# Kernel tuning notes

Hardware: AMD Instinct MI355X
Metric: run time of the kernel (lower is better)

Reference implementation:

```python
import jax, jax.numpy as jnp
import numpy as np

N_NODES = 100000
N_EDGES = 1000000
NEG_SLOPE = 0.2


def gat_conv(x, src, dst, W, al, ar, b, res, activation):
    """DGL-style GATConv. res is None (no residual), 'id' (identity residual), or a [in,H*D] matrix."""
    H, D = al.shape
    n = x.shape[0]
    feat = (x @ W).reshape(n, H, D)                      # [N,H,D]
    el = jnp.einsum('nhd,hd->nh', feat, al)              # [N,H]
    er = jnp.einsum('nhd,hd->nh', feat, ar)              # [N,H]
    e = jax.nn.leaky_relu(el[src] + er[dst], NEG_SLOPE)  # [E,H]
    # edge softmax over incoming edges of each dst node
    m = jax.lax.stop_gradient(jax.ops.segment_max(e, dst, num_segments=n))
    ex = jnp.exp(e - m[dst])
    s = jax.ops.segment_sum(ex, dst, num_segments=n)
    alpha = ex / s[dst]                                  # [E,H]
    out = jax.ops.segment_sum(feat[src] * alpha[:, :, None], dst, num_segments=n)  # [N,H,D]
    if res == 'id':
        out = out + x.reshape(n, H, D)
    elif res is not None:
        out = out + (x @ res).reshape(n, H, D)
    out = out + b.reshape(1, H, D)
    if activation is not None:
        out = activation(out)
    return out


def setup_inputs() -> dict:
    key = jax.random.key(0)
    ks = jax.random.split(key, 20)
    F_IN, HID = 128, 32
    H1, H2, H3 = 4, 4, 1
    C = 40
    sc = 0.1
    inp = {
        'x':   jax.random.normal(ks[0], (N_NODES, F_IN), dtype=jnp.float32),
        'src': jax.random.randint(ks[1], (N_EDGES,), 0, N_NODES, dtype=jnp.int32),
        'dst': jax.random.randint(ks[2], (N_EDGES,), 0, N_NODES, dtype=jnp.int32),
        # layer 1: in=128 -> H1*HID=128, no residual, elu
        'W1':  sc * jax.random.normal(ks[3], (F_IN, H1 * HID), dtype=jnp.float32),
        'al1': sc * jax.random.normal(ks[4], (H1, HID), dtype=jnp.float32),
        'ar1': sc * jax.random.normal(ks[5], (H1, HID), dtype=jnp.float32),
        'b1':  jnp.zeros((H1 * HID,), dtype=jnp.float32),
        # layer 2: in=128 -> H2*HID=128, identity residual, elu
        'W2':  sc * jax.random.normal(ks[6], (H1 * HID, H2 * HID), dtype=jnp.float32),
        'al2': sc * jax.random.normal(ks[7], (H2, HID), dtype=jnp.float32),
        'ar2': sc * jax.random.normal(ks[8], (H2, HID), dtype=jnp.float32),
        'b2':  jnp.zeros((H2 * HID,), dtype=jnp.float32),
        # layer 3 (output): in=128 -> H3*HID=32, projected residual, no activation
        'W3':  sc * jax.random.normal(ks[9], (H2 * HID, H3 * HID), dtype=jnp.float32),
        'al3': sc * jax.random.normal(ks[10], (H3, HID), dtype=jnp.float32),
        'ar3': sc * jax.random.normal(ks[11], (H3, HID), dtype=jnp.float32),
        'b3':  jnp.zeros((H3 * HID,), dtype=jnp.float32),
        'res3': sc * jax.random.normal(ks[12], (H2 * HID, H3 * HID), dtype=jnp.float32),
        # final classifier
        'Wfc': sc * jax.random.normal(ks[13], (HID, C), dtype=jnp.float32),
        'bfc': jnp.zeros((C,), dtype=jnp.float32),
    }
    return inp


def reference(x, src, dst, W1, al1, ar1, b1, W2, al2, ar2, b2, W3, al3, ar3, b3, res3, Wfc, bfc):
    n = x.shape[0]
    h = gat_conv(x, src, dst, W1, al1, ar1, b1, None, jax.nn.elu).reshape(n, -1)   # [N, 128]
    h = gat_conv(h, src, dst, W2, al2, ar2, b2, 'id', jax.nn.elu).reshape(n, -1)   # [N, 128]
    h = gat_conv(h, src, dst, W3, al3, ar3, b3, res3, None).mean(axis=1)           # [N, 32]
    return h @ Wfc + bfc                                                           # [N, 40]
```

## Files before the change

### kernel.cpp

```cpp
#include <hip/hip_runtime.h>
#include <cstdint>
#include <cstddef>

#define NN 100000
#define NE 1000000
#define GEMM_BLOCKS 1563
#define GEMM2_BLOCKS 782
#define TICKET4_BLOCKS 977
#define NB_SCAN 391
#define LOG2E 1.4426950408896340736f

typedef unsigned int uint;
typedef unsigned short ushort;
typedef __attribute__((ext_vector_type(8))) short bfrag;
typedef __attribute__((ext_vector_type(4))) float f32x4;

__device__ __forceinline__ ushort f2bf(float f){
  uint u = __float_as_uint(f);
  u += 0x7fffu + ((u >> 16) & 1u);
  return (ushort)(u >> 16);
}
__device__ __forceinline__ float bflo(uint p){ return __uint_as_float(p << 16); }
__device__ __forceinline__ float bfhi(uint p){ return __uint_as_float(p & 0xffff0000u); }


__device__ __forceinline__ void bfrag_body(const float* __restrict__ B1, const float* __restrict__ B2,
                                           int n1, int n2, int NT, ushort* __restrict__ out, int i){
  if (i >= NT*4*64) return;
  int l = i & 63, ks = (i>>6)&3, nt = i>>8;
  int col = nt*16 + (l&15);
  int k0  = ks*32 + (l>>4)*8;
  const float* B; int stride, c;
  if (col < n1){ B = B1; stride = n1; c = col; }
  else         { B = B2; stride = n2; c = col - n1; }
  ushort v[8];
  #pragma unroll
  for (int j=0;j<8;j++) v[j] = f2bf(B[(size_t)(k0+j)*stride + c]);
  uint4 pk;
  pk.x = (uint)v[0] | ((uint)v[1]<<16);
  pk.y = (uint)v[2] | ((uint)v[3]<<16);
  pk.z = (uint)v[4] | ((uint)v[5]<<16);
  pk.w = (uint)v[6] | ((uint)v[7]<<16);
  *(uint4*)(out + (size_t)i*8) = pk;
}

__global__ __launch_bounds__(256) void k_packs(const float* __restrict__ W1, const float* __restrict__ W2,
                                               const float* __restrict__ W3, const float* __restrict__ res3,
                                               ushort* __restrict__ Bf1, ushort* __restrict__ Bf2,
                                               ushort* __restrict__ Bf3){
  int r = blockIdx.x, t = threadIdx.x;
  if (r < 8)       bfrag_body(W1, nullptr, 128, 0, 8, Bf1, r*256 + t);
  else if (r < 16) bfrag_body(W2, nullptr, 128, 0, 8, Bf2, (r-8)*256 + t);
  else             bfrag_body(W3, res3,    32, 32, 4, Bf3, (r-16)*256 + t);
}


__global__ __launch_bounds__(256, 4)
void k_gemm1_ticket(const float* __restrict__ x, const ushort* __restrict__ Bf1,
                    ushort* __restrict__ featb,
                    const float* __restrict__ al, const float* __restrict__ ar,
                    float* __restrict__ el, float* __restrict__ er,
                    const int* __restrict__ dst, int* __restrict__ cnt4, int* __restrict__ tick){
  int bid = blockIdx.x, t = threadIdx.x;
  if (bid >= GEMM_BLOCKS){
    int idx = (bid - GEMM_BLOCKS)*256 + t;
    if (idx < NE/4){
      int e0 = idx*4;
      int4 d4 = *(const int4*)(dst + e0);
      int t0 = atomicAdd(&cnt4[(uint)d4.x*4u + 0u], 1);
      int t1 = atomicAdd(&cnt4[(uint)d4.y*4u + 1u], 1);
      int t2 = atomicAdd(&cnt4[(uint)d4.z*4u + 2u], 1);
      int t3 = atomicAdd(&cnt4[(uint)d4.w*4u + 3u], 1);
      *(int4*)(tick + e0) = make_int4(t0,t1,t2,t3);
    }
    return;
  }

  int l = t & 63, w = t >> 6;
  int rw = bid*64 + w*16;
  int c = l & 15, g = l >> 4;

  f32x4 acc[8];
  #pragma unroll
  for (int nt=0;nt<8;nt++) acc[nt] = (f32x4){0.f,0.f,0.f,0.f};

  int rowA = rw + c; if (rowA >= NN) rowA = NN-1;
  const float* Ap = x + (size_t)rowA*128 + g*8;
  const bfrag* Bp = (const bfrag*)Bf1;

  #pragma unroll
  for (int ks=0; ks<4; ++ks){
    float4 f0 = *(const float4*)(Ap + ks*32);
    float4 f1 = *(const float4*)(Ap + ks*32 + 4);
    bfrag a;
    a[0]=(short)f2bf(f0.x); a[1]=(short)f2bf(f0.y); a[2]=(short)f2bf(f0.z); a[3]=(short)f2bf(f0.w);
    a[4]=(short)f2bf(f1.x); a[5]=(short)f2bf(f1.y); a[6]=(short)f2bf(f1.z); a[7]=(short)f2bf(f1.w);
    #pragma unroll
    for (int nt=0; nt<8; ++nt){
      bfrag b = Bp[(nt*4+ks)*64 + l];
      acc[nt] = __builtin_amdgcn_mfma_f32_16x16x32_bf16(a, b, acc[nt], 0, 0, 0);
    }
  }

  float alv[4][2], arv[4][2];
  #pragma unroll
  for (int h=0;h<4;h++){
    alv[h][0]=al[h*32+c]*LOG2E;    arv[h][0]=ar[h*32+c]*LOG2E;
    alv[h][1]=al[h*32+16+c]*LOG2E; arv[h][1]=ar[h*32+16+c]*LOG2E;
  }

  #pragma unroll
  for (int reg=0; reg<4; ++reg){
    int row = rw + g*4 + reg;
    bool ok = row < NN;
    #pragma unroll
    for (int h=0;h<4;h++){
      float pl = acc[2*h][reg]*alv[h][0] + acc[2*h+1][reg]*alv[h][1];
      float pr = acc[2*h][reg]*arv[h][0] + acc[2*h+1][reg]*arv[h][1];
      #pragma unroll
      for (int off=1; off<16; off<<=1){ pl += __shfl_xor(pl,off); pr += __shfl_xor(pr,off); }
      if (ok && c==0){ el[(size_t)row*4 + h] = pl; er[(size_t)row*4 + h] = pr; }
    }
    if (ok){
      #pragma unroll
      for (int nt=0; nt<8; ++nt)
        featb[(size_t)row*128 + nt*16 + c] = f2bf(acc[nt][reg]);
    }
  }
}


__global__ __launch_bounds__(256) void k_scan_local(const int* __restrict__ cnt4, int* __restrict__ shoff,
                                                    int* __restrict__ rowptr, int* __restrict__ bsum){
  __shared__ int sm[256];
  int t = threadIdx.x;
  int i = blockIdx.x*256 + t;
  int v = 0;
  if (i < NN){
    int4 cc = ((const int4*)cnt4)[i];
    v = cc.x + cc.y + cc.z + cc.w;
    int4 so;
    so.x = 0; so.y = cc.x; so.z = cc.x + cc.y; so.w = cc.x + cc.y + cc.z;
    ((int4*)shoff)[i] = so;
  }
  sm[t] = v;
  __syncthreads();
  for (int off=1; off<256; off<<=1){
    int u = (t>=off) ? sm[t-off] : 0;
    __syncthreads();
    sm[t] += u;
    __syncthreads();
  }
  if (i < NN) rowptr[i] = sm[t] - v;
  if (t == 255) bsum[blockIdx.x] = sm[255];
}

__global__ __launch_bounds__(512) void k_scan_finish(int* __restrict__ rowptr, const int* __restrict__ bsum){
  __shared__ int sm[512];
  __shared__ int ex[512];
  int t = threadIdx.x;
  int v = (t < NB_SCAN) ? bsum[t] : 0;
  sm[t] = v;
  __syncthreads();
  for (int off=1; off<512; off<<=1){
    int u = (t>=off) ? sm[t-off] : 0;
    __syncthreads();
    sm[t] += u;
    __syncthreads();
  }
  ex[t] = sm[t] - v;
  __syncthreads();
  int i = blockIdx.x*512 + t;
  if (i < NN) rowptr[i] += ex[i>>8];
  else if (i == NN) rowptr[NN] = NE;
}


__global__ __launch_bounds__(256) void k_dhist(const int* __restrict__ rowptr, int* __restrict__ dbin){
  __shared__ int lh[256];
  int t = threadIdx.x;
  lh[t] = 0;
  __syncthreads();
  int n = blockIdx.x*256 + t;
  if (n < NN){
    int deg = rowptr[n+1] - rowptr[n];
    atomicAdd(&lh[deg > 255 ? 255 : deg], 1);
  }
  __syncthreads();
  if (lh[t] > 0) atomicAdd(&dbin[t], lh[t]);
}

__global__ __launch_bounds__(256) void k_dscan(int* __restrict__ dbin){
  __shared__ int sm[256];
  int t = threadIdx.x;
  int v = dbin[t];
  sm[t] = v;
  __syncthreads();
  for (int off=1; off<256; off<<=1){
    int u = (t>=off) ? sm[t-off] : 0;
    __syncthreads();
    sm[t] += u;
    __syncthreads();
  }
  dbin[t] = sm[t] - v;
}

__global__ __launch_bounds__(256) void k_place_dscat(const int* __restrict__ src, const int* __restrict__ dst,
                                                     const int* __restrict__ rowptr, const int* __restrict__ shoff,
                                                     const int* __restrict__ tick, int* __restrict__ csr,
                                                     int* __restrict__ dbin, int* __restrict__ perm){
  int bid = blockIdx.x, t = threadIdx.x;
  if (bid < TICKET4_BLOCKS){
    int idx = bid*256 + t;
    if (idx < NE/4){
      int e0 = idx*4;
      int4 s4 = *(const int4*)(src + e0);
      int4 d4 = *(const int4*)(dst + e0);
      int4 t4 = *(const int4*)(tick + e0);
      csr[rowptr[d4.x] + shoff[(uint)d4.x*4u + 0u] + t4.x] = s4.x;
      csr[rowptr[d4.y] + shoff[(uint)d4.y*4u + 1u] + t4.y] = s4.y;
      csr[rowptr[d4.z] + shoff[(uint)d4.z*4u + 2u] + t4.z] = s4.z;
      csr[rowptr[d4.w] + shoff[(uint)d4.w*4u + 3u] + t4.w] = s4.w;
    }
  } else {
    __shared__ int lh[256];
    __shared__ int lbase[256];
    lh[t] = 0;
    __syncthreads();
    int n = (bid - TICKET4_BLOCKS)*256 + t;
    int bin = -1, lticket = 0;
    if (n < NN){
      int deg = rowptr[n+1] - rowptr[n];
      bin = deg > 255 ? 255 : deg;
      lticket = atomicAdd(&lh[bin], 1);
    }
    __syncthreads();
    if (lh[t] > 0) lbase[t] = atomicAdd(&dbin[t], lh[t]);
    __syncthreads();
    if (n < NN) perm[lbase[bin] + lticket] = n;
  }
}


template<int NT, int NTF, int H>
__global__ __launch_bounds__(512) void k_gemm_mfma(const ushort* __restrict__ Ab, const ushort* __restrict__ Bf,
                                                   ushort* __restrict__ featb, float* __restrict__ Cres,
                                                   const float* __restrict__ al, const float* __restrict__ ar,
                                                   float* __restrict__ el, float* __restrict__ er, int M){
  __shared__ ushort Bs[NT*2048];
  int t = threadIdx.x;
  #pragma unroll
  for (int i=0; i<NT/2; ++i)
    ((uint4*)Bs)[i*512 + t] = ((const uint4*)Bf)[i*512 + t];
  __syncthreads();

  int l = t & 63, w = t >> 6;
  int rw = blockIdx.x*128 + w*16;
  int c = l & 15, g = l >> 4;

  f32x4 acc[NT];
  #pragma unroll
  for (int nt=0;nt<NT;nt++) acc[nt] = (f32x4){0.f,0.f,0.f,0.f};

  int rowA = rw + c; if (rowA >= M) rowA = M-1;
  const ushort* Ap = Ab + (size_t)rowA*128 + g*8;
  const bfrag* Bp = (const bfrag*)Bs;

  #pragma unroll
  for (int ks=0; ks<4; ++ks){
    bfrag a = *(const bfrag*)(Ap + ks*32);
    #pragma unroll
    for (int nt=0; nt<NT; ++nt){
      bfrag b = Bp[(nt*4+ks)*64 + l];
      acc[nt] = __builtin_amdgcn_mfma_f32_16x16x32_bf16(a, b, acc[nt], 0, 0, 0);
    }
  }

  float alv[H][2], arv[H][2];
  #pragma unroll
  for (int h=0;h<H;h++){
    alv[h][0]=al[h*32+c]*LOG2E;    arv[h][0]=ar[h*32+c]*LOG2E;
    alv[h][1]=al[h*32+16+c]*LOG2E; arv[h][1]=ar[h*32+16+c]*LOG2E;
  }

  #pragma unroll
  for (int reg=0; reg<4; ++reg){
    int row = rw + g*4 + reg;
    bool ok = row < M;
    #pragma unroll
    for (int h=0;h<H;h++){
      float pl = acc[2*h][reg]*alv[h][0] + acc[2*h+1][reg]*alv[h][1];
      float pr = acc[2*h][reg]*arv[h][0] + acc[2*h+1][reg]*arv[h][1];
      #pragma unroll
      for (int off=1; off<16; off<<=1){ pl += __shfl_xor(pl,off); pr += __shfl_xor(pr,off); }
      if (ok && c==0){ el[(size_t)row*H + h] = pl; er[(size_t)row*H + h] = pr; }
    }
    if (ok){
      #pragma unroll
      for (int nt=0; nt<NTF; ++nt)
        featb[(size_t)row*(NTF*16) + nt*16 + c] = f2bf(acc[nt][reg]);
      #pragma unroll
      for (int nt=NTF; nt<NT; ++nt)
        Cres[(size_t)row*((NT-NTF)*16) + (nt-NTF)*16 + c] = acc[nt][reg];
    }
  }
}


template<int RK>
__global__ __launch_bounds__(256) void k_agg4(const int* __restrict__ rowptr, const int* __restrict__ csr,
                                              const int* __restrict__ perm,
                                              const ushort* __restrict__ feat,
                                              const float* __restrict__ el, const float* __restrict__ er,
                                              const void* __restrict__ res, const float* __restrict__ bias,
                                              ushort* __restrict__ out, int act){
  int t = threadIdx.x;
  int l15 = t & 15;
  int node = perm[blockIdx.x*16 + (t>>4)];

  int beg = rowptr[node], deg = rowptr[node+1] - beg;
  int hm = l15 >> 2;
  float erh = er[(size_t)node*4 + hm];
  const int* cp = csr + beg;
  uint fo = (uint)l15*8u;

  float ssum = 0.f;
  float a0=0.f,a1=0.f,a2=0.f,a3=0.f,a4=0.f,a5=0.f,a6=0.f,a7=0.f;

  int ei = 0;
  for (; ei+4 <= deg; ei += 4){
    int s0 = cp[ei], s1 = cp[ei+1], s2 = cp[ei+2], s3 = cp[ei+3];
    uint4 p0 = *(const uint4*)(feat + ((uint)s0*128u + fo));
    uint4 p1 = *(const uint4*)(feat + ((uint)s1*128u + fo));
    uint4 p2 = *(const uint4*)(feat + ((uint)s2*128u + fo));
    uint4 p3 = *(const uint4*)(feat + ((uint)s3*128u + fo));
    float v0 = el[(uint)s0*4u + hm] + erh; v0 = fmaxf(v0, 0.2f*v0);
    float v1 = el[(uint)s1*4u + hm] + erh; v1 = fmaxf(v1, 0.2f*v1);
    float v2 = el[(uint)s2*4u + hm] + erh; v2 = fmaxf(v2, 0.2f*v2);
    float v3 = el[(uint)s3*4u + hm] + erh; v3 = fmaxf(v3, 0.2f*v3);
    float w0 = __builtin_amdgcn_exp2f(v0);
    float w1 = __builtin_amdgcn_exp2f(v1);
    float w2 = __builtin_amdgcn_exp2f(v2);
    float w3 = __builtin_amdgcn_exp2f(v3);
    ssum += (w0 + w1) + (w2 + w3);
    a0 += w0*bflo(p0.x) + w1*bflo(p1.x) + w2*bflo(p2.x) + w3*bflo(p3.x);
    a1 += w0*bfhi(p0.x) + w1*bfhi(p1.x) + w2*bfhi(p2.x) + w3*bfhi(p3.x);
    a2 += w0*bflo(p0.y) + w1*bflo(p1.y) + w2*bflo(p2.y) + w3*bflo(p3.y);
    a3 += w0*bfhi(p0.y) + w1*bfhi(p1.y) + w2*bfhi(p2.y) + w3*bfhi(p3.y);
    a4 += w0*bflo(p0.z) + w1*bflo(p1.z) + w2*bflo(p2.z) + w3*bflo(p3.z);
    a5 += w0*bfhi(p0.z) + w1*bfhi(p1.z) + w2*bfhi(p2.z) + w3*bfhi(p3.z);
    a6 += w0*bflo(p0.w) + w1*bflo(p1.w) + w2*bflo(p2.w) + w3*bflo(p3.w);
    a7 += w0*bfhi(p0.w) + w1*bfhi(p1.w) + w2*bfhi(p2.w) + w3*bfhi(p3.w);
  }
  for (; ei < deg; ++ei){
    int s0 = cp[ei];
    uint4 p0 = *(const uint4*)(feat + ((uint)s0*128u + fo));
    float v0 = el[(uint)s0*4u + hm] + erh; v0 = fmaxf(v0, 0.2f*v0);
    float w0 = __builtin_amdgcn_exp2f(v0);
    ssum += w0;
    a0 += w0*bflo(p0.x); a1 += w0*bfhi(p0.x);
    a2 += w0*bflo(p0.y); a3 += w0*bfhi(p0.y);
    a4 += w0*bflo(p0.z); a5 += w0*bfhi(p0.z);
    a6 += w0*bflo(p0.w); a7 += w0*bfhi(p0.w);
  }

  float inv = (deg > 0) ? 1.f/ssum : 0.f;
  float o0=a0*inv, o1=a1*inv, o2=a2*inv, o3=a3*inv;
  float o4=a4*inv, o5=a5*inv, o6=a6*inv, o7=a7*inv;
  if (RK == 1){
    uint4 rv = *(const uint4*)((const ushort*)res + (size_t)node*128 + fo);
    o0 += bflo(rv.x); o1 += bfhi(rv.x); o2 += bflo(rv.y); o3 += bfhi(rv.y);
    o4 += bflo(rv.z); o5 += bfhi(rv.z); o6 += bflo(rv.w); o7 += bfhi(rv.w);
  }
  float4 bv0 = *(const float4*)(bias + l15*8);
  float4 bv1 = *(const float4*)(bias + l15*8 + 4);
  o0 += bv0.x; o1 += bv0.y; o2 += bv0.z; o3 += bv0.w;
  o4 += bv1.x; o5 += bv1.y; o6 += bv1.z; o7 += bv1.w;
  if (act){
    o0 = (o0>0.f)?o0:__expf(o0)-1.f;
    o1 = (o1>0.f)?o1:__expf(o1)-1.f;
    o2 = (o2>0.f)?o2:__expf(o2)-1.f;
    o3 = (o3>0.f)?o3:__expf(o3)-1.f;
    o4 = (o4>0.f)?o4:__expf(o4)-1.f;
    o5 = (o5>0.f)?o5:__expf(o5)-1.f;
    o6 = (o6>0.f)?o6:__expf(o6)-1.f;
    o7 = (o7>0.f)?o7:__expf(o7)-1.f;
  }
  uint4 pk;
  pk.x = (uint)f2bf(o0) | ((uint)f2bf(o1)<<16);
  pk.y = (uint)f2bf(o2) | ((uint)f2bf(o3)<<16);
  pk.z = (uint)f2bf(o4) | ((uint)f2bf(o5)<<16);
  pk.w = (uint)f2bf(o6) | ((uint)f2bf(o7)<<16);
  *(uint4*)(out + (size_t)node*128 + fo) = pk;
}


__global__ __launch_bounds__(256) void k_agg1(const int* __restrict__ rowptr, const int* __restrict__ csr,
                                              const int* __restrict__ perm,
                                              const ushort* __restrict__ feat,
                                              const float* __restrict__ el, const float* __restrict__ er,
                                              const float* __restrict__ res, const float* __restrict__ bias,
                                              float* __restrict__ h3){
  int t = threadIdx.x;
  int l7 = t & 7;
  int node = perm[blockIdx.x*32 + (t>>3)];

  int beg = rowptr[node], deg = rowptr[node+1] - beg;
  float er0 = er[node];
  const int* cp = csr + beg;
  uint fo = (uint)l7*4u;

  float ssum = 0.f, a0=0.f, a1=0.f, a2=0.f, a3=0.f;
  int ei = 0;
  for (; ei+2 <= deg; ei += 2){
    int s0 = cp[ei], s1 = cp[ei+1];
    uint2 p0 = *(const uint2*)(feat + ((uint)s0*32u + fo));
    uint2 p1 = *(const uint2*)(feat + ((uint)s1*32u + fo));
    float v0 = el[s0] + er0; v0 = fmaxf(v0, 0.2f*v0);
    float v1 = el[s1] + er0; v1 = fmaxf(v1, 0.2f*v1);
    float w0 = __builtin_amdgcn_exp2f(v0);
    float w1 = __builtin_amdgcn_exp2f(v1);
    ssum += w0 + w1;
    a0 += w0*bflo(p0.x) + w1*bflo(p1.x);
    a1 += w0*bfhi(p0.x) + w1*bfhi(p1.x);
    a2 += w0*bflo(p0.y) + w1*bflo(p1.y);
    a3 += w0*bfhi(p0.y) + w1*bfhi(p1.y);
  }
  if (ei < deg){
    int s0 = cp[ei];
    uint2 p0 = *(const uint2*)(feat + ((uint)s0*32u + fo));
    float v0 = el[s0] + er0; v0 = fmaxf(v0, 0.2f*v0);
    float w0 = __builtin_amdgcn_exp2f(v0);
    ssum += w0;
    a0 += w0*bflo(p0.x); a1 += w0*bfhi(p0.x);
    a2 += w0*bflo(p0.y); a3 += w0*bfhi(p0.y);
  }

  float inv = (deg > 0) ? 1.f/ssum : 0.f;
  float4 rv = *(const float4*)(res + (size_t)node*32 + fo);
  float4 bv = *(const float4*)(bias + fo);
  float4 ov;
  ov.x = a0*inv + rv.x + bv.x;
  ov.y = a1*inv + rv.y + bv.y;
  ov.z = a2*inv + rv.z + bv.z;
  ov.w = a3*inv + rv.w + bv.w;
  *(float4*)(h3 + (size_t)node*32 + fo) = ov;
}


__global__ __launch_bounds__(256) void k_fc(const float* __restrict__ h, const float* __restrict__ W,
                                            const float* __restrict__ b, float* __restrict__ out){
  __shared__ float Ws[32*40];
  __shared__ float Hs[64][33];
  __shared__ float bs[40];
  int t = threadIdx.x;
  for (int i=t; i<1280; i+=256) Ws[i] = W[i];
  if (t < 40) bs[t] = b[t];
  int n0 = blockIdx.x*64;
  for (int idx=t; idx<512; idx+=256){
    int r = idx>>3, c4 = idx&7;
    float4 v;
    if (n0 + r < NN) v = *(const float4*)(h + (size_t)(n0+r)*32 + c4*4);
    else v = make_float4(0.f,0.f,0.f,0.f);
    Hs[r][c4*4+0]=v.x; Hs[r][c4*4+1]=v.y; Hs[r][c4*4+2]=v.z; Hs[r][c4*4+3]=v.w;
  }
  __syncthreads();
  int n = t>>2, cg = t&3;
  float acc[10];
  #pragma unroll
  for (int j=0;j<10;j++) acc[j] = 0.f;
  #pragma unroll
  for (int k=0;k<32;k++){
    float hv = Hs[n][k];
    #pragma unroll
    for (int j=0;j<10;j++) acc[j] += hv * Ws[k*40 + cg + 4*j];
  }
  int row = n0 + n;
  if (row < NN){
    #pragma unroll
    for (int j=0;j<10;j++) out[(size_t)row*40 + cg + 4*j] = acc[j] + bs[cg+4*j];
  }
}


extern "C" void kernel_launch(void* const* d_in, const int* in_sizes, int n_in,
                              void* d_out, int out_size, void* d_ws, size_t ws_size,
                              hipStream_t stream){
  const float* x    = (const float*)d_in[0];
  const int*   src  = (const int*)  d_in[1];
  const int*   dst  = (const int*)  d_in[2];
  const float* W1   = (const float*)d_in[3];
  const float* al1  = (const float*)d_in[4];
  const float* ar1  = (const float*)d_in[5];
  const float* b1   = (const float*)d_in[6];
  const float* W2   = (const float*)d_in[7];
  const float* al2  = (const float*)d_in[8];
  const float* ar2  = (const float*)d_in[9];
  const float* b2   = (const float*)d_in[10];
  const float* W3   = (const float*)d_in[11];
  const float* al3  = (const float*)d_in[12];
  const float* ar3  = (const float*)d_in[13];
  const float* b3   = (const float*)d_in[14];
  const float* res3 = (const float*)d_in[15];
  const float* Wfc  = (const float*)d_in[16];
  const float* bfc  = (const float*)d_in[17];
  float* out = (float*)d_out;

  char* ws = (char*)d_ws;
  size_t o = 0;
  auto alloc = [&](size_t bytes)->char*{
    char* p = ws + o;
    o += (bytes + 255) & ~(size_t)255;
    return p;
  };
  int*    rowptr = (int*)   alloc((size_t)(NN+1)*4);
  int*    cnt4   = (int*)   alloc((size_t)NN*4*4);
  int*    shoff  = (int*)   alloc((size_t)NN*4*4);
  int*    bsum   = (int*)   alloc(512*4);
  int*    dbin   = (int*)   alloc(256*4);
  int*    perm   = (int*)   alloc((size_t)NN*4);
  int*    tick   = (int*)   alloc((size_t)NE*4);
  int*    csr    = (int*)   alloc((size_t)NE*4);
  float*  el     = (float*) alloc((size_t)NN*4*4);
  float*  er     = (float*) alloc((size_t)NN*4*4);
  ushort* featb  = (ushort*)alloc((size_t)NN*128*2);
  ushort* h1b    = (ushort*)alloc((size_t)NN*128*2);
  ushort* h2b    = (ushort*)alloc((size_t)NN*128*2);
  float*  res3p  = (float*) alloc((size_t)NN*32*4);
  float*  h3     = (float*) alloc((size_t)NN*32*4);
  ushort* Bf1    = (ushort*)alloc((size_t)8*4*64*8*2);
  ushort* Bf2    = (ushort*)alloc((size_t)8*4*64*8*2);
  ushort* Bf3    = (ushort*)alloc((size_t)4*4*64*8*2);
  (void)ws_size; (void)n_in; (void)in_sizes; (void)out_size;

  hipMemsetAsync(cnt4, 0, (size_t)NN*4*4, stream);
  hipMemsetAsync(dbin, 0, 256*4, stream);

  k_packs<<<20, 256, 0, stream>>>(W1, W2, W3, res3, Bf1, Bf2, Bf3);

  k_gemm1_ticket<<<GEMM_BLOCKS+TICKET4_BLOCKS, 256, 0, stream>>>(x, Bf1, featb, al1, ar1, el, er,
                                                                 dst, cnt4, tick);

  k_scan_local<<<NB_SCAN, 256, 0, stream>>>(cnt4, shoff, rowptr, bsum);
  k_scan_finish<<<(NN+1+511)/512, 512, 0, stream>>>(rowptr, bsum);

  k_dhist<<<NB_SCAN, 256, 0, stream>>>(rowptr, dbin);
  k_dscan<<<1, 256, 0, stream>>>(dbin);
  k_place_dscat<<<TICKET4_BLOCKS+NB_SCAN, 256, 0, stream>>>(src, dst, rowptr, shoff, tick, csr,
                                                            dbin, perm);

  k_agg4<0><<<NN/16, 256, 0, stream>>>(rowptr, csr, perm, featb, el, er, nullptr, b1, h1b, 1);

  k_gemm_mfma<8,8,4><<<GEMM2_BLOCKS, 512, 0, stream>>>(h1b, Bf2, featb, nullptr, al2, ar2, el, er, NN);
  k_agg4<1><<<NN/16, 256, 0, stream>>>(rowptr, csr, perm, featb, el, er, h1b, b2, h2b, 1);

  k_gemm_mfma<4,2,1><<<GEMM2_BLOCKS, 512, 0, stream>>>(h2b, Bf3, featb, res3p, al3, ar3, el, er, NN);
  k_agg1<<<NN/32, 256, 0, stream>>>(rowptr, csr, perm, featb, el, er, res3p, b3, h3);
  k_fc<<<GEMM_BLOCKS, 256, 0, stream>>>(h3, Wfc, bfc, out);
}
```

Baseline: 298.0 us.

## Fold memsets and degree histogram into neighboring kernels, interleave ticket blocks with GEMM

Replaces the two memsets with zeroing blocks in the weight-packing kernel, and computes the degree histogram inside the local scan. The histogram scan runs as an extra block of the scan-finish kernel, removing four launches. The ticket-counting blocks are interleaved with the GEMM blocks and now handle one edge per thread instead of four, so atomics overlap with MFMA work. The risk is more blocks with less work each, and scalar dst loads in place of vectorized ones.

```diff
diff --git a/kernel.cpp b/kernel.cpp
--- a/kernel.cpp
+++ b/kernel.cpp
@@ -5,9 +5,12 @@
 #define NN 100000
 #define NE 1000000
 #define GEMM_BLOCKS 1563
+#define TICKET_BLOCKS 3907
+#define MERGED_BLOCKS 5470
 #define GEMM2_BLOCKS 782
 #define TICKET4_BLOCKS 977
 #define NB_SCAN 391
+#define NF_SCAN 196
 #define LOG2E 1.4426950408896340736f
 
 typedef unsigned int uint;
@@ -44,14 +47,21 @@
   *(uint4*)(out + (size_t)i*8) = pk;
 }
 
-__global__ __launch_bounds__(256) void k_packs(const float* __restrict__ W1, const float* __restrict__ W2,
+__global__ __launch_bounds__(256) void k_prep0(const float* __restrict__ W1, const float* __restrict__ W2,
                                                const float* __restrict__ W3, const float* __restrict__ res3,
                                                ushort* __restrict__ Bf1, ushort* __restrict__ Bf2,
-                                               ushort* __restrict__ Bf3){
+                                               ushort* __restrict__ Bf3,
+                                               int* __restrict__ cnt4, int* __restrict__ dbin){
   int r = blockIdx.x, t = threadIdx.x;
   if (r < 8)       bfrag_body(W1, nullptr, 128, 0, 8, Bf1, r*256 + t);
   else if (r < 16) bfrag_body(W2, nullptr, 128, 0, 8, Bf2, (r-8)*256 + t);
-  else             bfrag_body(W3, res3,    32, 32, 4, Bf3, (r-16)*256 + t);
+  else if (r < 20) bfrag_body(W3, res3,    32, 32, 4, Bf3, (r-16)*256 + t);
+  else if (r < 20 + NB_SCAN){
+    int i = (r-20)*256 + t;
+    if (i < NN) ((int4*)cnt4)[i] = make_int4(0,0,0,0);
+  } else {
+    dbin[t] = 0;
+  }
 }
 
 
@@ -61,20 +71,16 @@
                     const float* __restrict__ al, const float* __restrict__ ar,
                     float* __restrict__ el, float* __restrict__ er,
                     const int* __restrict__ dst, int* __restrict__ cnt4, int* __restrict__ tick){
-  int bid = blockIdx.x, t = threadIdx.x;
-  if (bid >= GEMM_BLOCKS){
-    int idx = (bid - GEMM_BLOCKS)*256 + t;
-    if (idx < NE/4){
-      int e0 = idx*4;
-      int4 d4 = *(const int4*)(dst + e0);
-      int t0 = atomicAdd(&cnt4[(uint)d4.x*4u + 0u], 1);
-      int t1 = atomicAdd(&cnt4[(uint)d4.y*4u + 1u], 1);
-      int t2 = atomicAdd(&cnt4[(uint)d4.z*4u + 2u], 1);
-      int t3 = atomicAdd(&cnt4[(uint)d4.w*4u + 3u], 1);
-      *(int4*)(tick + e0) = make_int4(t0,t1,t2,t3);
-    }
+  long b = blockIdx.x;
+  int t = threadIdx.x;
+  int g_lo = (int)( b      * GEMM_BLOCKS / MERGED_BLOCKS);
+  int g_hi = (int)((b + 1) * GEMM_BLOCKS / MERGED_BLOCKS);
+  if (g_hi == g_lo){
+    int e = (int)(b - g_lo)*256 + t;
+    if (e < NE) tick[e] = atomicAdd(&cnt4[(uint)dst[e]*4u + (e & 3)], 1);
     return;
   }
+  int bid = g_lo;
 
   int l = t & 63, w = t >> 6;
   int rw = bid*64 + w*16;
@@ -97,8 +103,8 @@
     a[4]=(short)f2bf(f1.x); a[5]=(short)f2bf(f1.y); a[6]=(short)f2bf(f1.z); a[7]=(short)f2bf(f1.w);
     #pragma unroll
     for (int nt=0; nt<8; ++nt){
-      bfrag b = Bp[(nt*4+ks)*64 + l];
-      acc[nt] = __builtin_amdgcn_mfma_f32_16x16x32_bf16(a, b, acc[nt], 0, 0, 0);
+      bfrag bb = Bp[(nt*4+ks)*64 + l];
+      acc[nt] = __builtin_amdgcn_mfma_f32_16x16x32_bf16(a, bb, acc[nt], 0, 0, 0);
     }
   }
 
@@ -131,9 +137,12 @@
 
 
 __global__ __launch_bounds__(256) void k_scan_local(const int* __restrict__ cnt4, int* __restrict__ shoff,
-                                                    int* __restrict__ rowptr, int* __restrict__ bsum){
+                                                    int* __restrict__ rowptr, int* __restrict__ bsum,
+                                                    int* __restrict__ dbin){
   __shared__ int sm[256];
-  int t = threadIdx.x;
+  __shared__ int lh[256];
+  int t = threadIdx.x;
+  lh[t] = 0;
   int i = blockIdx.x*256 + t;
   int v = 0;
   if (i < NN){
@@ -145,6 +154,7 @@
   }
   sm[t] = v;
   __syncthreads();
+  if (i < NN) atomicAdd(&lh[v > 255 ? 255 : v], 1);
   for (int off=1; off<256; off<<=1){
     int u = (t>=off) ? sm[t-off] : 0;
     __syncthreads();
@@ -153,12 +163,29 @@
   }
   if (i < NN) rowptr[i] = sm[t] - v;
   if (t == 255) bsum[blockIdx.x] = sm[255];
-}
-
-__global__ __launch_bounds__(512) void k_scan_finish(int* __restrict__ rowptr, const int* __restrict__ bsum){
+  __syncthreads();
+  if (lh[t] > 0) atomicAdd(&dbin[t], lh[t]);
+}
+
+
+__global__ __launch_bounds__(512) void k_scan_finish(int* __restrict__ rowptr, const int* __restrict__ bsum,
+                                                     int* __restrict__ dbin){
   __shared__ int sm[512];
+  int t = threadIdx.x;
+  if (blockIdx.x == NF_SCAN){
+    int v = (t < 256) ? dbin[t] : 0;
+    sm[t] = v;
+    __syncthreads();
+    for (int off=1; off<512; off<<=1){
+      int u = (t>=off) ? sm[t-off] : 0;
+      __syncthreads();
+      sm[t] += u;
+      __syncthreads();
+    }
+    if (t < 256) dbin[t] = sm[t] - v;
+    return;
+  }
   __shared__ int ex[512];
-  int t = threadIdx.x;
   int v = (t < NB_SCAN) ? bsum[t] : 0;
   sm[t] = v;
   __syncthreads();
@@ -175,35 +202,6 @@
   else if (i == NN) rowptr[NN] = NE;
 }
 
-
-__global__ __launch_bounds__(256) void k_dhist(const int* __restrict__ rowptr, int* __restrict__ dbin){
-  __shared__ int lh[256];
-  int t = threadIdx.x;
-  lh[t] = 0;
-  __syncthreads();
-  int n = blockIdx.x*256 + t;
-  if (n < NN){
-    int deg = rowptr[n+1] - rowptr[n];
-    atomicAdd(&lh[deg > 255 ? 255 : deg], 1);
-  }
-  __syncthreads();
-  if (lh[t] > 0) atomicAdd(&dbin[t], lh[t]);
-}
-
-__global__ __launch_bounds__(256) void k_dscan(int* __restrict__ dbin){
-  __shared__ int sm[256];
-  int t = threadIdx.x;
-  int v = dbin[t];
-  sm[t] = v;
-  __syncthreads();
-  for (int off=1; off<256; off<<=1){
-    int u = (t>=off) ? sm[t-off] : 0;
-    __syncthreads();
-    sm[t] += u;
-    __syncthreads();
-  }
-  dbin[t] = sm[t] - v;
-}
 
 __global__ __launch_bounds__(256) void k_place_dscat(const int* __restrict__ src, const int* __restrict__ dst,
                                                      const int* __restrict__ rowptr, const int* __restrict__ shoff,
@@ -533,19 +531,14 @@
   ushort* Bf3    = (ushort*)alloc((size_t)4*4*64*8*2);
   (void)ws_size; (void)n_in; (void)in_sizes; (void)out_size;
 
-  hipMemsetAsync(cnt4, 0, (size_t)NN*4*4, stream);
-  hipMemsetAsync(dbin, 0, 256*4, stream);
-
-  k_packs<<<20, 256, 0, stream>>>(W1, W2, W3, res3, Bf1, Bf2, Bf3);
-
-  k_gemm1_ticket<<<GEMM_BLOCKS+TICKET4_BLOCKS, 256, 0, stream>>>(x, Bf1, featb, al1, ar1, el, er,
-                                                                 dst, cnt4, tick);
-
-  k_scan_local<<<NB_SCAN, 256, 0, stream>>>(cnt4, shoff, rowptr, bsum);
-  k_scan_finish<<<(NN+1+511)/512, 512, 0, stream>>>(rowptr, bsum);
-
-  k_dhist<<<NB_SCAN, 256, 0, stream>>>(rowptr, dbin);
-  k_dscan<<<1, 256, 0, stream>>>(dbin);
+  k_prep0<<<20+NB_SCAN+1, 256, 0, stream>>>(W1, W2, W3, res3, Bf1, Bf2, Bf3, cnt4, dbin);
+
+  k_gemm1_ticket<<<MERGED_BLOCKS, 256, 0, stream>>>(x, Bf1, featb, al1, ar1, el, er,
+                                                    dst, cnt4, tick);
+
+  k_scan_local<<<NB_SCAN, 256, 0, stream>>>(cnt4, shoff, rowptr, bsum, dbin);
+  k_scan_finish<<<NF_SCAN+1, 512, 0, stream>>>(rowptr, bsum, dbin);
+
   k_place_dscat<<<TICKET4_BLOCKS+NB_SCAN, 256, 0, stream>>>(src, dst, rowptr, shoff, tick, csr,
                                                             dbin, perm);
 
```

Result: faster. 274.2 us, median of 3 (-8.0%).
